# Kernel optimization log

Hardware: AMD Instinct MI355X
Metric: run time of the kernel (lower is better)

Reference implementation:

```python
import jax, jax.numpy as jnp
import numpy as np

LN_EPS = 1e-5


def layer_norm(x, g, b):
    m = jnp.mean(x, axis=-1, keepdims=True)
    v = jnp.mean(jnp.square(x - m), axis=-1, keepdims=True)
    return (x - m) * jax.lax.rsqrt(v + LN_EPS) * g + b


def sym_norm(A):
    # D^{-1/2} (A + I) D^{-1/2}
    N = A.shape[0]
    Ah = A + jnp.eye(N, dtype=A.dtype)
    d = jnp.sum(Ah, axis=-1)
    dinv = jax.lax.rsqrt(jnp.maximum(d, 1e-12))
    return Ah * dinv[:, None] * dinv[None, :]


def gru_layer(xs, Wih, Whh, bih, bhh):
    # xs: (BN, T, Din) -> ys: (BN, T, H). PyTorch GRU cell math.
    BN, T, _ = xs.shape
    H = Whh.shape[1]
    x_proj = xs @ Wih.T + bih  # (BN, T, 3H), precompute input projections

    def step(h, xp):
        hp = h @ Whh.T + bhh
        xr, xz, xn = jnp.split(xp, 3, axis=-1)
        hr, hz, hn = jnp.split(hp, 3, axis=-1)
        r = jax.nn.sigmoid(xr + hr)
        z = jax.nn.sigmoid(xz + hz)
        n = jnp.tanh(xn + r * hn)
        h_new = (1.0 - z) * n + z * h
        return h_new, h_new

    h0 = jnp.zeros((BN, H), xs.dtype)
    _, ys = jax.lax.scan(step, h0, jnp.swapaxes(x_proj, 0, 1))
    return jnp.swapaxes(ys, 0, 1)


def amscf_forward(x, A, FSP, DSP,
                  E1, E2, fus_W, fus_b, fus_v, beta1, beta2,
                  gcn_W1, gcn_b1, ln1_g, ln1_b, gcn_W2, gcn_b2, ln2_g, ln2_b,
                  gru_Wih0, gru_Whh0, gru_bih0, gru_bhh0,
                  gru_Wih1, gru_Whh1, gru_bih1, gru_bhh1,
                  att_w, fc1_W, fc1_b, fc2_W, fc2_b):
    B, T, N, _ = x.shape
    Hor = fc2_W.shape[0]

    # ImprovedAdjacency: blend A with adaptive node-embedding adjacency
    Aadp = jax.nn.softmax(jax.nn.relu(E1 @ E2.T), axis=-1)
    IA = 0.5 * A + 0.5 * Aadp

    # fuse_with_A with learned gates
    w1 = jax.nn.sigmoid(beta1)
    w2 = jax.nn.sigmoid(beta2)
    C1 = w1 * A + (1.0 - w1) * FSP
    C2 = w2 * A + (1.0 - w2) * DSP

    # TransposeAttentionFusion: graph-level attention over the 3 candidate graphs
    Gs = jnp.stack([IA, C1, C2], axis=0)  # (3, N, N)
    sc = jnp.mean(jnp.tanh(Gs @ fus_W.T + fus_b) @ fus_v, axis=-1)  # (3,)
    alpha = jax.nn.softmax(sc)
    MG = jnp.einsum('k,knm->nm', alpha, Gs)

    S_hat = sym_norm(MG)  # (N, N)

    # TwoLayerGCN over all (B, T) at once: act(LN(S X W1)) -> LN(S h W2)
    xf = x.reshape(B * T, N, 1)
    h = jnp.einsum('mn,bnc->bmc', S_hat, xf) @ gcn_W1 + gcn_b1
    h = jax.nn.relu(layer_norm(h, ln1_g, ln1_b))
    g = jnp.einsum('mn,bnc->bmc', S_hat, h) @ gcn_W2 + gcn_b2
    g = layer_norm(g, ln2_g, ln2_b)  # (B*T, N, C)

    C = g.shape[-1]
    # Faithful to original: raw view of (B, T, N, C) into (B*N, T, C)
    H_seq = g.reshape(B, T, N, C).reshape(B * N, T, C)

    out = gru_layer(H_seq, gru_Wih0, gru_Whh0, gru_bih0, gru_bhh0)
    out = gru_layer(out, gru_Wih1, gru_Whh1, gru_bih1, gru_bhh1)  # (BN, T, Hg)

    # SoftAttentionPooling over time
    score = out @ att_w  # (BN, T)
    att = jax.nn.softmax(score, axis=1)
    ctx = jnp.einsum('bt,bth->bh', att, out)

    hfc = jax.nn.gelu(ctx @ fc1_W.T + fc1_b)
    dlt = hfc @ fc2_W.T + fc2_b  # (BN, Hor); dropout is identity at eval
    return jnp.transpose(dlt.reshape(B, N, Hor), (0, 2, 1))  # (B, Hor, N)


def setup_inputs() -> dict:
    B, T, N, Hor = 32, 12, 1000, 12
    Cin, Ch, Cout, Hg, Da, De = 1, 96, 96, 192, 32, 10
    key = jax.random.key(0)
    ks = jax.random.split(key, 32)
    f32 = jnp.float32

    def nrm(k, shape, scale):
        return jax.random.normal(k, shape, dtype=f32) * scale

    inp = {
        'x': jax.random.normal(ks[0], (B, T, N, Cin), dtype=f32),
        'A': jax.random.uniform(ks[1], (N, N), dtype=f32),
        'FSP': jax.random.uniform(ks[2], (N, N), dtype=f32),
        'DSP': jax.random.uniform(ks[3], (N, N), dtype=f32),
        'E1': nrm(ks[4], (N, De), 0.1),
        'E2': nrm(ks[5], (N, De), 0.1),
        'fus_W': nrm(ks[6], (Da, N), 1.0 / np.sqrt(N)),
        'fus_b': jnp.zeros((Da,), f32),
        'fus_v': nrm(ks[7], (Da,), 1.0 / np.sqrt(Da)),
        'beta1': jnp.float32(0.5),
        'beta2': jnp.float32(0.5),
        'gcn_W1': nrm(ks[8], (Cin, Ch), 1.0 / np.sqrt(Cin)),
        'gcn_b1': jnp.zeros((Ch,), f32),
        'ln1_g': jnp.ones((Ch,), f32),
        'ln1_b': jnp.zeros((Ch,), f32),
        'gcn_W2': nrm(ks[9], (Ch, Cout), 1.0 / np.sqrt(Ch)),
        'gcn_b2': jnp.zeros((Cout,), f32),
        'ln2_g': jnp.ones((Cout,), f32),
        'ln2_b': jnp.zeros((Cout,), f32),
        'gru_Wih0': nrm(ks[10], (3 * Hg, Cout), 1.0 / np.sqrt(Hg)),
        'gru_Whh0': nrm(ks[11], (3 * Hg, Hg), 1.0 / np.sqrt(Hg)),
        'gru_bih0': jnp.zeros((3 * Hg,), f32),
        'gru_bhh0': jnp.zeros((3 * Hg,), f32),
        'gru_Wih1': nrm(ks[12], (3 * Hg, Hg), 1.0 / np.sqrt(Hg)),
        'gru_Whh1': nrm(ks[13], (3 * Hg, Hg), 1.0 / np.sqrt(Hg)),
        'gru_bih1': jnp.zeros((3 * Hg,), f32),
        'gru_bhh1': jnp.zeros((3 * Hg,), f32),
        'att_w': nrm(ks[14], (Hg,), 1.0 / np.sqrt(Hg)),
        'fc1_W': nrm(ks[15], (Hg, Hg), 1.0 / np.sqrt(Hg)),
        'fc1_b': jnp.zeros((Hg,), f32),
        'fc2_W': nrm(ks[16], (Hor, Hg), 1.0 / np.sqrt(Hg)),
        'fc2_b': jnp.zeros((Hor,), f32),
    }
    return inp


def reference(x, A, FSP, DSP, E1, E2, fus_W, fus_b, fus_v, beta1, beta2,
              gcn_W1, gcn_b1, ln1_g, ln1_b, gcn_W2, gcn_b2, ln2_g, ln2_b,
              gru_Wih0, gru_Whh0, gru_bih0, gru_bhh0,
              gru_Wih1, gru_Whh1, gru_bih1, gru_bhh1,
              att_w, fc1_W, fc1_b, fc2_W, fc2_b):
    return amscf_forward(x, A, FSP, DSP, E1, E2, fus_W, fus_b, fus_v, beta1, beta2,
                         gcn_W1, gcn_b1, ln1_g, ln1_b, gcn_W2, gcn_b2, ln2_g, ln2_b,
                         gru_Wih0, gru_Whh0, gru_bih0, gru_bhh0,
                         gru_Wih1, gru_Whh1, gru_bih1, gru_bhh1,
                         att_w, fc1_W, fc1_b, fc2_W, fc2_b)
```

## Files before the change

kernel.cpp:

```cpp
#include <hip/hip_runtime.h>

typedef unsigned short u16;
typedef unsigned int u32;
typedef __attribute__((ext_vector_type(8))) short short8;
typedef __attribute__((ext_vector_type(4))) float float4v;

#define DEV static __device__ __forceinline__

DEV float bf2f(u16 u) { u32 x = ((u32)u) << 16; float f; __builtin_memcpy(&f, &x, 4); return f; }
DEV u16 f2bf(float f) {
  u32 u; __builtin_memcpy(&u, &f, 4);
  u = (u + 0x7fffu + ((u >> 16) & 1u)) >> 16;
  return (u16)u;
}
DEV float sigm(float x) { return 1.f / (1.f + __expf(-x)); }

DEV void gl16(const u16* g, u16* l) {
  __builtin_amdgcn_global_load_lds(
      (const __attribute__((address_space(1))) void*)g,
      (__attribute__((address_space(3))) void*)l, 16, 0, 0);
}

template <int OMODE>
__launch_bounds__(256)
__global__ void gemm_nt(const u16* __restrict__ A, int lda,
                        const u16* __restrict__ B, int ldb,
                        void* __restrict__ Cp, int ldc,
                        int M, int N, int K,
                        const float* __restrict__ bias)
{
  constexpr int PK = 40;
  __shared__ u16 As[128 * PK];
  __shared__ u16 Bs[64 * PK];

  const int tid  = threadIdx.x;
  const int m0   = blockIdx.y * 128;
  const int n0   = blockIdx.x * 64;
  const int wid  = tid >> 6;
  const int lane = tid & 63;
  const int l15  = lane & 15;
  const int quad = lane >> 4;
  const int wm   = (wid >> 1) * 64;
  const int wn   = (wid & 1) * 32;

  float4v acc[4][2];
  const float4v fz = {0.f, 0.f, 0.f, 0.f};
#pragma unroll
  for (int i = 0; i < 4; i++)
#pragma unroll
    for (int j = 0; j < 2; j++) acc[i][j] = fz;

  const int arow = tid >> 2;
  const int akc  = tid & 3;

  const int kt_count = (K + 31) / 32;
  for (int kt = 0; kt < kt_count; ++kt) {
    const int k0 = kt * 32 + akc * 8;
    const bool kok = (k0 < K);
    uint4 av0 = make_uint4(0, 0, 0, 0), av1 = av0, bv = av0;
    int ra = m0 + arow;
    if (kok && ra < M)        av0 = *(const uint4*)(A + (size_t)ra * lda + k0);
    if (kok && ra + 64 < M)   av1 = *(const uint4*)(A + (size_t)(ra + 64) * lda + k0);
    int rb = n0 + arow;
    if (kok && rb < N)        bv  = *(const uint4*)(B + (size_t)rb * ldb + k0);

    __syncthreads();
    *(uint4*)&As[arow * PK + akc * 8]        = av0;
    *(uint4*)&As[(arow + 64) * PK + akc * 8] = av1;
    *(uint4*)&Bs[arow * PK + akc * 8]        = bv;
    __syncthreads();

    short8 af[4], bfr[2];
#pragma unroll
    for (int i = 0; i < 4; i++)
      af[i] = *(const short8*)&As[(wm + i * 16 + l15) * PK + quad * 8];
#pragma unroll
    for (int j = 0; j < 2; j++)
      bfr[j] = *(const short8*)&Bs[(wn + j * 16 + l15) * PK + quad * 8];
#pragma unroll
    for (int i = 0; i < 4; i++)
#pragma unroll
      for (int j = 0; j < 2; j++)
        acc[i][j] = __builtin_amdgcn_mfma_f32_16x16x32_bf16(af[i], bfr[j], acc[i][j], 0, 0, 0);
  }

#pragma unroll
  for (int i = 0; i < 4; i++)
#pragma unroll
    for (int j = 0; j < 2; j++)
#pragma unroll
      for (int e = 0; e < 4; e++) {
        int r = m0 + wm + i * 16 + quad * 4 + e;
        int c = n0 + wn + j * 16 + l15;
        if (r < M && c < N) {
          float v = acc[i][j][e];
          if (OMODE == 0) ((float*)Cp)[(size_t)r * ldc + c] = v;
          else {
            float a = v + bias[c];
            float t = tanhf(0.7978845608028654f * (a + 0.044715f * a * a * a));
            ((float*)Cp)[(size_t)r * ldc + c] = 0.5f * a * (1.f + t);
          }
        }
      }
}

__launch_bounds__(256)
__global__ void k_bigemm(const u16* __restrict__ A,
                         const u16* __restrict__ B,
                         u16* __restrict__ Gg)
{
  __shared__ u16 As[128 * 32];
  __shared__ u16 Bs[128 * 32];
  const int tid  = threadIdx.x;
  const int bid  = blockIdx.x;
  const int xcd  = bid & 7;
  const int jj   = bid >> 3;
  const int m0   = (jj & 7) * 128;
  const int n0   = (xcd + 8 * (jj >> 3)) * 128;

  const int wid  = tid >> 6;
  const int lane = tid & 63;
  const int l15  = lane & 15;
  const int quad = lane >> 4;
  const int wm   = (wid >> 1) * 64;
  const int wn   = (wid & 1) * 64;

  const int srow = wid * 16 + (lane >> 2);
  const int skc  = (lane & 3) * 8;

  const u16* agp0 = A + (size_t)(m0 + srow) * 1024 + skc;
  const u16* agp1 = agp0 + (size_t)64 * 1024;
  const u16* bgp0 = B + (size_t)(n0 + srow) * 1024 + skc;
  const u16* bgp1 = bgp0 + (size_t)64 * 1024;
  u16* asl0 = &As[(wid * 16) * 32];
  u16* asl1 = &As[(64 + wid * 16) * 32];
  u16* bsl0 = &Bs[(wid * 16) * 32];
  u16* bsl1 = &Bs[(64 + wid * 16) * 32];

  float4v acc[4][4];
  const float4v fz = {0.f, 0.f, 0.f, 0.f};
#pragma unroll
  for (int i = 0; i < 4; i++)
#pragma unroll
    for (int j = 0; j < 4; j++) acc[i][j] = fz;

  for (int kt = 0; kt < 32; ++kt) {
    const int ko = kt * 32;
    gl16(agp0 + ko, asl0);
    gl16(agp1 + ko, asl1);
    gl16(bgp0 + ko, bsl0);
    gl16(bgp1 + ko, bsl1);
    __syncthreads();
    short8 af[4], bf[4];
#pragma unroll
    for (int i = 0; i < 4; i++)
      af[i] = *(const short8*)&As[(wm + i * 16 + l15) * 32 + quad * 8];
#pragma unroll
    for (int j = 0; j < 4; j++)
      bf[j] = *(const short8*)&Bs[(wn + j * 16 + l15) * 32 + quad * 8];
#pragma unroll
    for (int i = 0; i < 4; i++)
#pragma unroll
      for (int j = 0; j < 4; j++)
        acc[i][j] = __builtin_amdgcn_mfma_f32_16x16x32_bf16(af[i], bf[j], acc[i][j], 0, 0, 0);
    __syncthreads();
  }

#pragma unroll
  for (int i = 0; i < 4; i++)
#pragma unroll
    for (int j = 0; j < 4; j++)
#pragma unroll
      for (int e = 0; e < 4; e++) {
        int r = m0 + wm + i * 16 + quad * 4 + e;
        if (r < 1000) {
          int c = n0 + wn + j * 16 + l15;
          int rs = c / 96, cc = c - rs * 96;
          Gg[(size_t)rs * 96000 + (size_t)r * 96 + cc] = f2bf(acc[i][j][e]);
        }
      }
}

template <int KX, bool POOL>
__launch_bounds__(256)
__global__ void k_gru(const u16* __restrict__ Xin, int ldx,
                      const u16* __restrict__ Win,
                      const u16* __restrict__ Hin,
                      const u16* __restrict__ Whh,
                      const float* __restrict__ bih, const float* __restrict__ bhh,
                      u16* __restrict__ Hout,
                      const float* __restrict__ att_w, float* __restrict__ score,
                      int t0)
{
  __shared__ u16 As[128 * 32];
  __shared__ u16 Bs[96 * 32];
  const int tid  = threadIdx.x;
  const int m0   = blockIdx.y * 128;
  const int c0   = blockIdx.x * 32;
  const int wid  = tid >> 6;
  const int lane = tid & 63;
  const int l15  = lane & 15;
  const int quad = lane >> 4;
  const int wm   = wid * 32;
  const int srow = lane >> 2;
  const int skc  = (lane & 3) * 8;

  float4v aR[2][2], aZ[2][2], aXN[2][2], aHN[2][2];
  const float4v fz = {0.f, 0.f, 0.f, 0.f};
#pragma unroll
  for (int i = 0; i < 2; i++)
#pragma unroll
    for (int j = 0; j < 2; j++) { aR[i][j] = fz; aZ[i][j] = fz; aXN[i][j] = fz; aHN[i][j] = fz; }

  const int br0   = wid * 16 + srow;
  const int grow0 = (br0 >> 5) * 192 + c0 + (br0 & 31);
  const int br1   = 64 + wid * 16 + srow;
  const int grow1 = 384 + c0 + (br1 & 31);
  u16* asl0 = &As[(wid * 16) * 32];
  u16* asl1 = &As[(64 + wid * 16) * 32];
  u16* bsl0 = &Bs[(wid * 16) * 32];
  u16* bsl1 = &Bs[(64 + wid * 16) * 32];

  {
    const u16* ax0 = Xin + (size_t)(m0 + wid * 16 + srow) * ldx + skc;
    const u16* ax1 = Xin + (size_t)(m0 + 64 + wid * 16 + srow) * ldx + skc;
    const u16* bx0 = Win + (size_t)grow0 * KX + skc;
    const u16* bx1 = Win + (size_t)grow1 * KX + skc;
#pragma unroll
    for (int kt = 0; kt < KX / 32; ++kt) {
      const int ko = kt * 32;
      gl16(ax0 + ko, asl0); gl16(ax1 + ko, asl1);
      gl16(bx0 + ko, bsl0);
      if (wid < 2) gl16(bx1 + ko, bsl1);
      __syncthreads();
      short8 af[2], bR[2], bZ[2], bN[2];
#pragma unroll
      for (int i = 0; i < 2; i++)
        af[i] = *(const short8*)&As[(wm + i * 16 + l15) * 32 + quad * 8];
#pragma unroll
      for (int j = 0; j < 2; j++) {
        bR[j] = *(const short8*)&Bs[(j * 16 + l15) * 32 + quad * 8];
        bZ[j] = *(const short8*)&Bs[(32 + j * 16 + l15) * 32 + quad * 8];
        bN[j] = *(const short8*)&Bs[(64 + j * 16 + l15) * 32 + quad * 8];
      }
#pragma unroll
      for (int i = 0; i < 2; i++)
#pragma unroll
        for (int j = 0; j < 2; j++) {
          aR[i][j]  = __builtin_amdgcn_mfma_f32_16x16x32_bf16(af[i], bR[j], aR[i][j], 0, 0, 0);
          aZ[i][j]  = __builtin_amdgcn_mfma_f32_16x16x32_bf16(af[i], bZ[j], aZ[i][j], 0, 0, 0);
          aXN[i][j] = __builtin_amdgcn_mfma_f32_16x16x32_bf16(af[i], bN[j], aXN[i][j], 0, 0, 0);
        }
      __syncthreads();
    }
  }
  if (!t0) {
    const u16* ah0 = Hin + (size_t)(m0 + wid * 16 + srow) * 192 + skc;
    const u16* ah1 = Hin + (size_t)(m0 + 64 + wid * 16 + srow) * 192 + skc;
    const u16* bh0 = Whh + (size_t)grow0 * 192 + skc;
    const u16* bh1 = Whh + (size_t)grow1 * 192 + skc;
#pragma unroll
    for (int kt = 0; kt < 6; ++kt) {
      const int ko = kt * 32;
      gl16(ah0 + ko, asl0); gl16(ah1 + ko, asl1);
      gl16(bh0 + ko, bsl0);
      if (wid < 2) gl16(bh1 + ko, bsl1);
      __syncthreads();
      short8 af[2], bR[2], bZ[2], bN[2];
#pragma unroll
      for (int i = 0; i < 2; i++)
        af[i] = *(const short8*)&As[(wm + i * 16 + l15) * 32 + quad * 8];
#pragma unroll
      for (int j = 0; j < 2; j++) {
        bR[j] = *(const short8*)&Bs[(j * 16 + l15) * 32 + quad * 8];
        bZ[j] = *(const short8*)&Bs[(32 + j * 16 + l15) * 32 + quad * 8];
        bN[j] = *(const short8*)&Bs[(64 + j * 16 + l15) * 32 + quad * 8];
      }
#pragma unroll
      for (int i = 0; i < 2; i++)
#pragma unroll
        for (int j = 0; j < 2; j++) {
          aR[i][j]  = __builtin_amdgcn_mfma_f32_16x16x32_bf16(af[i], bR[j], aR[i][j], 0, 0, 0);
          aZ[i][j]  = __builtin_amdgcn_mfma_f32_16x16x32_bf16(af[i], bZ[j], aZ[i][j], 0, 0, 0);
          aHN[i][j] = __builtin_amdgcn_mfma_f32_16x16x32_bf16(af[i], bN[j], aHN[i][j], 0, 0, 0);
        }
      __syncthreads();
    }
  }

  float ps[2][4];
  if (POOL) {
#pragma unroll
    for (int i = 0; i < 2; i++)
#pragma unroll
      for (int e = 0; e < 4; e++) ps[i][e] = 0.f;
  }
#pragma unroll
  for (int j = 0; j < 2; ++j) {
    const int c = c0 + j * 16 + l15;
    const float brz = bih[c] + bhh[c];
    const float bzz = bih[192 + c] + bhh[192 + c];
    const float bxn = bih[384 + c];
    const float bhn = bhh[384 + c];
    const float aw  = POOL ? att_w[c] : 0.f;
#pragma unroll
    for (int i = 0; i < 2; ++i)
#pragma unroll
      for (int e = 0; e < 4; ++e) {
        const int row = m0 + wm + i * 16 + quad * 4 + e;
        float rg  = sigm(aR[i][j][e] + brz);
        float zg  = sigm(aZ[i][j][e] + bzz);
        float hnv = bhn + (t0 ? 0.f : aHN[i][j][e]);
        float ng  = tanhf(aXN[i][j][e] + bxn + rg * hnv);
        float hold = t0 ? 0.f : bf2f(Hin[(size_t)row * 192 + c]);
        float hnew = (1.f - zg) * ng + zg * hold;
        Hout[(size_t)row * 192 + c] = f2bf(hnew);
        if (POOL) ps[i][e] += hnew * aw;
      }
  }
  if (POOL) {
#pragma unroll
    for (int i = 0; i < 2; ++i)
#pragma unroll
      for (int e = 0; e < 4; ++e) {
        float v = ps[i][e];
        v += __shfl_xor(v, 1); v += __shfl_xor(v, 2);
        v += __shfl_xor(v, 4); v += __shfl_xor(v, 8);
        if (l15 == 0) atomicAdd(&score[m0 + wm + i * 16 + quad * 4 + e], v);
      }
  }
}

__launch_bounds__(256)
__global__ void k_pool(const u16* __restrict__ H, float* __restrict__ score,
                       float* __restrict__ Mbuf, float* __restrict__ Lbuf,
                       float* __restrict__ Nv, int t0)
{
  const int base = blockIdx.x * 1536;
  const int tid  = threadIdx.x;

  float prev[6], hnew[6], so[6], wn[6];
#pragma unroll
  for (int k = 0; k < 6; k++) {
    const int idx = base + tid + k * 256;
    const int q = idx / 192;
    const float s = score[q];
    hnew[k] = bf2f(H[idx]);
    if (t0) {
      so[k] = 0.f; wn[k] = 1.f; prev[k] = 0.f;
    } else {
      const float Mo = Mbuf[q];
      const float Mn = fmaxf(Mo, s);
      so[k] = __expf(Mo - Mn);
      wn[k] = __expf(s - Mn);
      prev[k] = Nv[idx];
    }
  }
  float Mw = 0.f, Lw = 0.f;
  int qw = -1;
  if (tid < 8) {
    qw = blockIdx.x * 8 + tid;
    const float s = score[qw];
    if (t0) { Mw = s; Lw = 1.f; }
    else {
      const float Mo = Mbuf[qw];
      const float Mn = fmaxf(Mo, s);
      Mw = Mn;
      Lw = Lbuf[qw] * __expf(Mo - Mn) + __expf(s - Mn);
    }
  }
  __syncthreads();
  if (tid < 8) { Mbuf[qw] = Mw; Lbuf[qw] = Lw; score[qw] = 0.f; }
#pragma unroll
  for (int k = 0; k < 6; k++) {
    const int idx = base + tid + k * 256;
    Nv[idx] = prev[k] * so[k] + wn[k] * hnew[k];
  }
}

__launch_bounds__(256)
__global__ void k_h2gemm(const float* __restrict__ yt, const float4* __restrict__ cwpk,
                         const u16* __restrict__ W2s, const float* __restrict__ consts,
                         u16* __restrict__ h2t)
{
  constexpr int PK = 40;
  __shared__ u16 As[128 * PK];
  __shared__ u16 Bs[96 * PK];
  __shared__ u16 Ts[96 * 136];

  const int tid  = threadIdx.x;
  const int m0   = blockIdx.x * 128;
  const int wid  = tid >> 6;
  const int lane = tid & 63;
  const int l15  = lane & 15;
  const int quad = lane >> 4;
  const int wm   = (wid >> 1) * 64;
  const int wn   = (wid & 1) * 48;

  const float P = consts[0], Q = consts[1], VW = consts[2], CWB = consts[3], VB = consts[4];

  const int arow = tid >> 2;
  const int akc  = tid & 3;

  float yv[2], mu[2], iv[2];
#pragma unroll
  for (int rr = 0; rr < 2; rr++) {
    int i = m0 + arow + rr * 64;
    int r = i / 1000, n = i - r * 1000;
    float y = yt[n * 384 + r];
    yv[rr] = y;
    mu[rr] = y * P + Q;
    iv[rr] = rsqrtf(y * y * VW + 2.f * y * CWB + VB + 1e-5f);
  }

  float4v acc[4][3];
  const float4v fz = {0.f, 0.f, 0.f, 0.f};
#pragma unroll
  for (int i = 0; i < 4; i++)
#pragma unroll
    for (int j = 0; j < 3; j++) acc[i][j] = fz;

  uint4 asave[2][3];
  const bool has2 = (arow < 32);

  for (int kt = 0; kt < 6; ++kt) {
    const int k0 = kt * 32 + akc * 8;
    uint4 av[2];
    if (kt < 3) {
#pragma unroll
      for (int rr = 0; rr < 2; rr++) {
        u16 hb[8];
#pragma unroll
        for (int e = 0; e < 8; e++) {
          float4 cw = cwpk[k0 + e];
          float t = yv[rr] * cw.x + cw.y - mu[rr];
          float h = fmaxf(t * iv[rr] * cw.z + cw.w, 0.f);
          hb[e] = f2bf(h);
        }
        __builtin_memcpy(&av[rr], hb, 16);
        asave[rr][kt] = av[rr];
      }
    } else {
      av[0] = asave[0][kt - 3];
      av[1] = asave[1][kt - 3];
    }
    uint4 bv0 = *(const uint4*)(W2s + (size_t)arow * 192 + k0);
    uint4 bv1 = make_uint4(0, 0, 0, 0);
    if (has2) bv1 = *(const uint4*)(W2s + (size_t)(arow + 64) * 192 + k0);

    __syncthreads();
    *(uint4*)&As[arow * PK + akc * 8]        = av[0];
    *(uint4*)&As[(arow + 64) * PK + akc * 8] = av[1];
    *(uint4*)&Bs[arow * PK + akc * 8]        = bv0;
    if (has2) *(uint4*)&Bs[(arow + 64) * PK + akc * 8] = bv1;
    __syncthreads();

    short8 af[4], bfr[3];
#pragma unroll
    for (int i = 0; i < 4; i++)
      af[i] = *(const short8*)&As[(wm + i * 16 + l15) * PK + quad * 8];
#pragma unroll
    for (int j = 0; j < 3; j++)
      bfr[j] = *(const short8*)&Bs[(wn + j * 16 + l15) * PK + quad * 8];
#pragma unroll
    for (int i = 0; i < 4; i++)
#pragma unroll
      for (int j = 0; j < 3; j++)
        acc[i][j] = __builtin_amdgcn_mfma_f32_16x16x32_bf16(af[i], bfr[j], acc[i][j], 0, 0, 0);
  }

#pragma unroll
  for (int i = 0; i < 4; i++)
#pragma unroll
    for (int j = 0; j < 3; j++)
#pragma unroll
      for (int e = 0; e < 4; e++) {
        int rowl = wm + i * 16 + quad * 4 + e;
        int c2   = wn + j * 16 + l15;
        Ts[c2 * 136 + rowl] = f2bf(acc[i][j][e]);
      }
  __syncthreads();
#pragma unroll
  for (int u = tid; u < 1536; u += 256) {
    int c2 = u >> 4, ch = u & 15;
    int iidx0 = m0 + ch * 8;
    int r = iidx0 / 1000, n0 = iidx0 - r * 1000;
    *(uint4*)(h2t + (size_t)(r * 96 + c2) * 1024 + n0) = *(const uint4*)&Ts[c2 * 136 + ch * 8];
  }
}

__launch_bounds__(256)
__global__ void k_prep(const float* x, const float* fus_W,
                       const float* Wih0, const float* Whh0,
                       const float* Wih1, const float* Whh1,
                       const float* gcn_W1, const float* gcn_b1,
                       const float* gcn_W2, const float* ln1g, const float* ln1b,
                       u16* xbf, u16* fusWbf, u16* Wih0b, u16* Whh0b, u16* Wih1b, u16* Whh1b,
                       u16* W2s, float4* cwpk, float* consts)
{
  long o = (long)blockIdx.x * 256 + threadIdx.x;
  if (o < 384000) xbf[o] = f2bf(x[o]);
  else if ((o -= 384000) < 32000) fusWbf[o] = f2bf(fus_W[o]);
  else if ((o -= 32000) < 55296)  Wih0b[o] = f2bf(Wih0[o]);
  else if ((o -= 55296) < 110592) Whh0b[o] = f2bf(Whh0[o]);
  else if ((o -= 110592) < 110592) Wih1b[o] = f2bf(Wih1[o]);
  else if ((o -= 110592) < 110592) Whh1b[o] = f2bf(Whh1[o]);
  else if ((o -= 110592) < 9216) {
    int c2 = (int)o / 96, c = (int)o - c2 * 96;
    float wv = gcn_W2[c * 96 + c2];
    u16 hi = f2bf(wv);
    u16 lo = f2bf(wv - bf2f(hi));
    W2s[c2 * 192 + c] = hi;
    W2s[c2 * 192 + 96 + c] = lo;
  }
  else if ((o -= 9216) < 96) {
    int c = (int)o;
    float4 cw;
    cw.x = gcn_W1[c]; cw.y = gcn_b1[c]; cw.z = ln1g[c]; cw.w = ln1b[c];
    cwpk[c] = cw;
  }
  if (blockIdx.x == 0 && threadIdx.x == 0) {
    float sw = 0, sb = 0, sww = 0, swb = 0, sbb = 0;
    for (int c = 0; c < 96; c++) {
      float wv = gcn_W1[c], b = gcn_b1[c];
      sw += wv; sb += b; sww += wv * wv; swb += wv * b; sbb += b * b;
    }
    float P = sw / 96.f, Q = sb / 96.f;
    consts[0] = P; consts[1] = Q;
    consts[2] = sww / 96.f - P * P;
    consts[3] = swb / 96.f - P * Q;
    consts[4] = sbb / 96.f - Q * Q;
  }
}

__launch_bounds__(256)
__global__ void k_zero(u16* __restrict__ h2t, float* __restrict__ score)
{
  int idx = blockIdx.x * 256 + threadIdx.x;
  if (idx < 110592) {
    int row = idx / 3, p = idx - row * 3;
    *(uint4*)(h2t + (size_t)row * 1024 + 1000 + p * 8) = make_uint4(0, 0, 0, 0);
  } else if ((idx -= 110592) < 32000) {
    score[idx] = 0.f;
  }
}

__launch_bounds__(256)
__global__ void k_w1split(const float* __restrict__ fc1W, u16* __restrict__ w1s)
{
  int idx = blockIdx.x * 256 + threadIdx.x;
  if (idx >= 192 * 192) return;
  int n = idx / 192, k = idx - n * 192;
  float w = fc1W[idx];
  u16 hi = f2bf(w);
  u16 lo = f2bf(w - bf2f(hi));
  w1s[(size_t)n * 576 + k]       = hi;
  w1s[(size_t)n * 576 + 192 + k] = lo;
  w1s[(size_t)n * 576 + 384 + k] = hi;
}

__launch_bounds__(256)
__global__ void k_adjrow(const float* __restrict__ A, const float* __restrict__ FSP,
                         const float* __restrict__ DSP, const float* __restrict__ E1,
                         const float* __restrict__ E2,
                         const float* beta1, const float* beta2,
                         u16* __restrict__ G, float* __restrict__ rowsums)
{
  __shared__ float z[1000];
  __shared__ float red[256];
  const int n = blockIdx.x, tid = threadIdx.x;

  float e1r[10];
#pragma unroll
  for (int d = 0; d < 10; d++) e1r[d] = E1[n * 10 + d];

  float lmax = -1e30f;
  for (int m = tid; m < 1000; m += 256) {
    float s = 0;
#pragma unroll
    for (int d = 0; d < 10; d++) s += e1r[d] * E2[m * 10 + d];
    s = fmaxf(s, 0.f);
    z[m] = s;
    lmax = fmaxf(lmax, s);
  }
  red[tid] = lmax; __syncthreads();
  for (int st = 128; st > 0; st >>= 1) { if (tid < st) red[tid] = fmaxf(red[tid], red[tid + st]); __syncthreads(); }
  const float mx = red[0]; __syncthreads();

  float lsum = 0;
  for (int m = tid; m < 1000; m += 256) { float e = __expf(z[m] - mx); z[m] = e; lsum += e; }
  red[tid] = lsum; __syncthreads();
  for (int st = 128; st > 0; st >>= 1) { if (tid < st) red[tid] += red[tid + st]; __syncthreads(); }
  const float inv = 1.f / red[0]; __syncthreads();

  const float w1 = sigm(beta1[0]);
  const float w2 = sigm(beta2[0]);
  float s0 = 0, s1 = 0, s2 = 0;
  for (int m = tid; m < 1000; m += 256) {
    float aadp = z[m] * inv;
    float a = A[n * 1000 + m], f = FSP[n * 1000 + m], dd = DSP[n * 1000 + m];
    float g0 = 0.5f * a + 0.5f * aadp;
    float g1 = w1 * a + (1.f - w1) * f;
    float g2 = w2 * a + (1.f - w2) * dd;
    G[0 * 1000000 + n * 1000 + m] = f2bf(g0);
    G[1 * 1000000 + n * 1000 + m] = f2bf(g1);
    G[2 * 1000000 + n * 1000 + m] = f2bf(g2);
    s0 += g0; s1 += g1; s2 += g2;
  }
  red[tid] = s0; __syncthreads();
  for (int st = 128; st > 0; st >>= 1) { if (tid < st) red[tid] += red[tid + st]; __syncthreads(); }
  if (tid == 0) rowsums[n] = red[0];
  __syncthreads();
  red[tid] = s1; __syncthreads();
  for (int st = 128; st > 0; st >>= 1) { if (tid < st) red[tid] += red[tid + st]; __syncthreads(); }
  if (tid == 0) rowsums[1000 + n] = red[0];
  __syncthreads();
  red[tid] = s2; __syncthreads();
  for (int st = 128; st > 0; st >>= 1) { if (tid < st) red[tid] += red[tid + st]; __syncthreads(); }
  if (tid == 0) rowsums[2000 + n] = red[0];
}

__launch_bounds__(256)
__global__ void k_sc(const float* __restrict__ P, const float* fus_b, const float* fus_v, float* sc)
{
  __shared__ float red[256];
  const int k = blockIdx.x, tid = threadIdx.x;
  float local = 0;
  for (int n = tid; n < 1000; n += 256) {
    const float* p = P + (size_t)(k * 1000 + n) * 32;
    float s = 0;
#pragma unroll
    for (int a = 0; a < 32; a++) s += tanhf(p[a] + fus_b[a]) * fus_v[a];
    local += s;
  }
  red[tid] = local; __syncthreads();
  for (int st = 128; st > 0; st >>= 1) { if (tid < st) red[tid] += red[tid + st]; __syncthreads(); }
  if (tid == 0) sc[k] = red[0] * (1.f / 1000.f);
}

__launch_bounds__(256)
__global__ void k_alpha(const float* sc, const float* rowsums, float* alpha_out, float* dinv)
{
  __shared__ float al[3];
  const int tid = threadIdx.x;
  if (tid == 0) {
    float m = fmaxf(sc[0], fmaxf(sc[1], sc[2]));
    float e0 = __expf(sc[0] - m), e1 = __expf(sc[1] - m), e2 = __expf(sc[2] - m);
    float inv = 1.f / (e0 + e1 + e2);
    al[0] = e0 * inv; al[1] = e1 * inv; al[2] = e2 * inv;
    alpha_out[0] = al[0]; alpha_out[1] = al[1]; alpha_out[2] = al[2];
  }
  __syncthreads();
  const float a0 = al[0], a1 = al[1], a2 = al[2];
  for (int n = tid; n < 1000; n += 256) {
    float d = a0 * rowsums[n] + a1 * rowsums[1000 + n] + a2 * rowsums[2000 + n] + 1.0f;
    dinv[n] = rsqrtf(fmaxf(d, 1e-12f));
  }
}

__launch_bounds__(256)
__global__ void k_shat(const u16* __restrict__ G, const float* alpha, const float* dinv,
                       u16* __restrict__ S)
{
  int idx = blockIdx.x * 256 + threadIdx.x;
  if (idx >= 1024000) return;
  int i = idx >> 10, j = idx & 1023;
  u16 val = 0;
  if (j < 1000) {
    const float a0 = alpha[0], a1 = alpha[1], a2 = alpha[2];
    int g = i * 1000 + j;
    float mg = a0 * bf2f(G[g]) + a1 * bf2f(G[1000000 + g]) + a2 * bf2f(G[2000000 + g]);
    if (i == j) mg += 1.0f;
    val = f2bf(mg * dinv[i] * dinv[j]);
  }
  S[(size_t)i * 1024 + j] = val;
}

__launch_bounds__(256)
__global__ void k_ln2g(u16* __restrict__ g, const float* __restrict__ b2,
                       const float* __restrict__ g2, const float* __restrict__ be2)
{
  const int i = blockIdx.x * 256 + threadIdx.x;
  if (i >= 384000) return;
  u16* row = g + (size_t)i * 96;

  uint4 raw[12];
#pragma unroll
  for (int t = 0; t < 12; t++) raw[t] = *(const uint4*)((const u16*)row + t * 8);

  float s = 0, ss = 0;
#pragma unroll
  for (int t = 0; t < 12; t++) {
    const u16* ch = (const u16*)&raw[t];
#pragma unroll
    for (int e = 0; e < 8; e++) {
      float v = bf2f(ch[e]) + b2[t * 8 + e];
      s += v; ss += v * v;
    }
  }
  const float mean = s * (1.f / 96.f);
  const float var  = ss * (1.f / 96.f) - mean * mean;
  const float isd  = rsqrtf(var + 1e-5f);

#pragma unroll
  for (int t = 0; t < 12; t++) {
    const u16* ch = (const u16*)&raw[t];
#pragma unroll
    for (int p = 0; p < 2; p++) {
      int c0 = t * 8 + p * 4;
      u32 w0 = f2bf((bf2f(ch[p * 4 + 0]) + b2[c0 + 0] - mean) * isd * g2[c0 + 0] + be2[c0 + 0]);
      u32 w1 = f2bf((bf2f(ch[p * 4 + 1]) + b2[c0 + 1] - mean) * isd * g2[c0 + 1] + be2[c0 + 1]);
      u32 w2 = f2bf((bf2f(ch[p * 4 + 2]) + b2[c0 + 2] - mean) * isd * g2[c0 + 2] + be2[c0 + 2]);
      u32 w3 = f2bf((bf2f(ch[p * 4 + 3]) + b2[c0 + 3] - mean) * isd * g2[c0 + 3] + be2[c0 + 3]);
      ((u32*)row)[t * 4 + p * 2 + 0] = (w0 | (w1 << 16));
      ((u32*)row)[t * 4 + p * 2 + 1] = (w2 | (w3 << 16));
    }
  }
}

__launch_bounds__(256)
__global__ void k_ctxsplit(const float* __restrict__ Nv, const float* __restrict__ Lbuf,
                           u16* __restrict__ ctxs)
{
  const int i = blockIdx.x * 256 + threadIdx.x;
  if (i >= 32000 * 192) return;
  const int q = i / 192, c = i - q * 192;
  float v = Nv[i] / Lbuf[q];
  u16 hi = f2bf(v);
  u16 lo = f2bf(v - bf2f(hi));
  u16* row = ctxs + (size_t)q * 576;
  row[c] = hi; row[192 + c] = hi; row[384 + c] = lo;
}

__launch_bounds__(192)
__global__ void k_fc2(const float* __restrict__ hfc, const float* __restrict__ fc2W,
                      const float* __restrict__ fc2b, float* __restrict__ out)
{
  __shared__ float w2S[12][193];
  __shared__ float hS[16][193];
  const int tid = threadIdx.x;
  const int q0 = blockIdx.x * 16;
  for (int idx = tid; idx < 12 * 192; idx += 192) {
    int o = idx / 192, k = idx - o * 192;
    w2S[o][k] = fc2W[idx];
  }
  for (int idx = tid; idx < 16 * 192; idx += 192) {
    int qq = idx / 192, k = idx - qq * 192;
    hS[qq][k] = hfc[(size_t)(q0 + qq) * 192 + k];
  }
  __syncthreads();
  const int qq = tid / 12, o = tid - qq * 12;
  float acc = fc2b[o];
#pragma unroll 8
  for (int k = 0; k < 192; k++) acc += hS[qq][k] * w2S[o][k];
  const int q = q0 + qq;
  const int b = q / 1000, node = q - b * 1000;
  out[(size_t)b * 12000 + o * 1000 + node] = acc;
}

extern "C" void kernel_launch(void* const* d_in, const int* in_sizes, int n_in,
                              void* d_out, int out_size, void* d_ws, size_t ws_size,
                              hipStream_t stream)
{
  const float* x     = (const float*)d_in[0];
  const float* A     = (const float*)d_in[1];
  const float* FSP   = (const float*)d_in[2];
  const float* DSP   = (const float*)d_in[3];
  const float* E1    = (const float*)d_in[4];
  const float* E2    = (const float*)d_in[5];
  const float* fus_W = (const float*)d_in[6];
  const float* fus_b = (const float*)d_in[7];
  const float* fus_v = (const float*)d_in[8];
  const float* beta1 = (const float*)d_in[9];
  const float* beta2 = (const float*)d_in[10];
  const float* gcn_W1= (const float*)d_in[11];
  const float* gcn_b1= (const float*)d_in[12];
  const float* ln1g  = (const float*)d_in[13];
  const float* ln1b  = (const float*)d_in[14];
  const float* gcn_W2= (const float*)d_in[15];
  const float* gcn_b2= (const float*)d_in[16];
  const float* ln2g  = (const float*)d_in[17];
  const float* ln2b  = (const float*)d_in[18];
  const float* Wih0  = (const float*)d_in[19];
  const float* Whh0  = (const float*)d_in[20];
  const float* bih0  = (const float*)d_in[21];
  const float* bhh0  = (const float*)d_in[22];
  const float* Wih1  = (const float*)d_in[23];
  const float* Whh1  = (const float*)d_in[24];
  const float* bih1  = (const float*)d_in[25];
  const float* bhh1  = (const float*)d_in[26];
  const float* att_w = (const float*)d_in[27];
  const float* fc1W  = (const float*)d_in[28];
  const float* fc1b  = (const float*)d_in[29];
  const float* fc2W  = (const float*)d_in[30];
  const float* fc2b  = (const float*)d_in[31];
  float* out = (float*)d_out;

  char* w = (char*)d_ws;
  auto alloc = [&](size_t bytes) -> char* {
    char* p = w;
    w += (bytes + 255) & ~(size_t)255;
    return p;
  };

  float* consts  = (float*)alloc(8 * 4);
  float* scp     = (float*)alloc(3 * 4);
  float* alphap  = (float*)alloc(3 * 4);
  float* rowsums = (float*)alloc(3000 * 4);
  float* dinvp   = (float*)alloc(1000 * 4);
  u16*   Gbuf    = (u16*)alloc((size_t)3000000 * 2);
  u16*   Sbf     = (u16*)alloc((size_t)1024 * 1024 * 2);
  u16*   xbf     = (u16*)alloc((size_t)384000 * 2);
  u16*   fusWbf  = (u16*)alloc((size_t)32000 * 2);
  u16*   Wih0b   = (u16*)alloc((size_t)55296 * 2);
  u16*   Whh0b   = (u16*)alloc((size_t)110592 * 2);
  u16*   Wih1b   = (u16*)alloc((size_t)110592 * 2);
  u16*   Whh1b   = (u16*)alloc((size_t)110592 * 2);
  u16*   w1s     = (u16*)alloc((size_t)192 * 576 * 2);
  u16*   W2s     = (u16*)alloc((size_t)96 * 192 * 2);
  float4* cwpk   = (float4*)alloc((size_t)96 * 16);
  float* Pbuf    = (float*)alloc((size_t)96000 * 4);
  float* yt      = (float*)alloc((size_t)384000 * 4);
  u16*   h2t     = (u16*)alloc((size_t)36864 * 1024 * 2);
  u16*   Gg      = (u16*)alloc((size_t)36864000 * 2);
  float* Nv      = (float*)alloc((size_t)6144000 * 4);
  float* Mbuf    = (float*)alloc((size_t)32000 * 4);
  float* Lbuf    = (float*)alloc((size_t)32000 * 4);
  float* score   = (float*)alloc((size_t)32000 * 4);

  u16* h0buf[2] = { h2t,                    h2t + (size_t)6144000 };
  u16* h1buf[2] = { h2t + (size_t)12288000, h2t + (size_t)18432000 };
  u16*   ctxs = h2t;
  float* hfc  = (float*)(h2t + (size_t)18432000);

  k_prep<<<3174, 256, 0, stream>>>(x, fus_W, Wih0, Whh0, Wih1, Whh1, gcn_W1, gcn_b1,
                                   gcn_W2, ln1g, ln1b,
                                   xbf, fusWbf, Wih0b, Whh0b, Wih1b, Whh1b, W2s, cwpk, consts);
  k_w1split<<<144, 256, 0, stream>>>(fc1W, w1s);
  k_zero<<<557, 256, 0, stream>>>(h2t, score);
  k_adjrow<<<1000, 256, 0, stream>>>(A, FSP, DSP, E1, E2, beta1, beta2, Gbuf, rowsums);
  gemm_nt<0><<<dim3(1, 24), 256, 0, stream>>>(Gbuf, 1000, fusWbf, 1000, Pbuf, 32, 3000, 32, 1000, nullptr);
  k_sc<<<3, 256, 0, stream>>>(Pbuf, fus_b, fus_v, scp);
  k_alpha<<<1, 256, 0, stream>>>(scp, rowsums, alphap, dinvp);
  k_shat<<<4000, 256, 0, stream>>>(Gbuf, alphap, dinvp, Sbf);
  gemm_nt<0><<<dim3(6, 8), 256, 0, stream>>>(Sbf, 1024, xbf, 1000, yt, 384, 1000, 384, 1000, nullptr);
  k_h2gemm<<<3000, 256, 0, stream>>>(yt, cwpk, W2s, consts, h2t);
  k_bigemm<<<2304, 256, 0, stream>>>(Sbf, h2t, Gg);
  k_ln2g<<<1500, 256, 0, stream>>>(Gg, gcn_b2, ln2g, ln2b);

  for (int t = 0; t < 12; ++t) {
    u16* h0in  = h0buf[t & 1];
    u16* h0out = h0buf[(t & 1) ^ 1];
    u16* h1in  = h1buf[t & 1];
    u16* h1out = h1buf[(t & 1) ^ 1];
    k_gru<96, false><<<dim3(6, 250), 256, 0, stream>>>(
        Gg + t * 96, 1152, Wih0b, h0in, Whh0b, bih0, bhh0, h0out, nullptr, nullptr, t == 0);
    k_gru<192, true><<<dim3(6, 250), 256, 0, stream>>>(
        h0out, 192, Wih1b, h1in, Whh1b, bih1, bhh1, h1out, att_w, score, t == 0);
    k_pool<<<4000, 256, 0, stream>>>(h1out, score, Mbuf, Lbuf, Nv, t == 0);
  }

  k_ctxsplit<<<24000, 256, 0, stream>>>(Nv, Lbuf, ctxs);
  gemm_nt<3><<<dim3(3, 250), 256, 0, stream>>>(ctxs, 576, w1s, 576, hfc, 192, 32000, 192, 576, fc1b);
  k_fc2<<<2000, 192, 0, stream>>>(hfc, fc2W, fc2b, out);
}
```

Baseline: 1.651 ms.

## Swizzle LDS tiles and widen GRU K-tiles to 64 to cut bank conflicts

Applies an XOR swizzle to the LDS column placement in the big GEMM and in the GRU kernel, so the MFMA fragment reads spread across banks instead of conflicting. For the 192-wide inputs and the hidden-state GEMMs in the GRU, the K tile grows from 32 to 64 with an 8-way swizzle. This halves the number of barrier-separated load stages, at the cost of larger LDS buffers, which may reduce occupancy. The GRU step kernel is launched once per timestep, so per-step latency dominates the total time.

```diff
diff --git a/kernel.cpp b/kernel.cpp
--- a/kernel.cpp
+++ b/kernel.cpp
@@ -126,7 +126,7 @@
   const int wn   = (wid & 1) * 64;
 
   const int srow = wid * 16 + (lane >> 2);
-  const int skc  = (lane & 3) * 8;
+  const int skc  = (((lane & 3) ^ ((lane >> 2) & 3))) * 8;
 
   const u16* agp0 = A + (size_t)(m0 + srow) * 1024 + skc;
   const u16* agp1 = agp0 + (size_t)64 * 1024;
@@ -144,6 +144,8 @@
 #pragma unroll
     for (int j = 0; j < 4; j++) acc[i][j] = fz;
 
+  const int swa = (quad ^ (l15 & 3)) * 8;
+
   for (int kt = 0; kt < 32; ++kt) {
     const int ko = kt * 32;
     gl16(agp0 + ko, asl0);
@@ -154,10 +156,10 @@
     short8 af[4], bf[4];
 #pragma unroll
     for (int i = 0; i < 4; i++)
-      af[i] = *(const short8*)&As[(wm + i * 16 + l15) * 32 + quad * 8];
+      af[i] = *(const short8*)&As[(wm + i * 16 + l15) * 32 + swa];
 #pragma unroll
     for (int j = 0; j < 4; j++)
-      bf[j] = *(const short8*)&Bs[(wn + j * 16 + l15) * 32 + quad * 8];
+      bf[j] = *(const short8*)&Bs[(wn + j * 16 + l15) * 32 + swa];
 #pragma unroll
     for (int i = 0; i < 4; i++)
 #pragma unroll
@@ -192,8 +194,8 @@
                       const float* __restrict__ att_w, float* __restrict__ score,
                       int t0)
 {
-  __shared__ u16 As[128 * 32];
-  __shared__ u16 Bs[96 * 32];
+  __shared__ u16 As[128 * 64];
+  __shared__ u16 Bs[96 * 64];
   const int tid  = threadIdx.x;
   const int m0   = blockIdx.y * 128;
   const int c0   = blockIdx.x * 32;
@@ -202,8 +204,11 @@
   const int l15  = lane & 15;
   const int quad = lane >> 4;
   const int wm   = wid * 32;
-  const int srow = lane >> 2;
-  const int skc  = (lane & 3) * 8;
+
+  const int srow8 = lane >> 3;
+  const int sw8   = ((lane & 7) ^ srow8) * 8;
+  const int srow4 = lane >> 2;
+  const int sw4   = (((lane & 3) ^ (srow4 & 3))) * 8;
 
   float4v aR[2][2], aZ[2][2], aXN[2][2], aHN[2][2];
   const float4v fz = {0.f, 0.f, 0.f, 0.f};
@@ -212,22 +217,20 @@
 #pragma unroll
     for (int j = 0; j < 2; j++) { aR[i][j] = fz; aZ[i][j] = fz; aXN[i][j] = fz; aHN[i][j] = fz; }
 
-  const int br0   = wid * 16 + srow;
-  const int grow0 = (br0 >> 5) * 192 + c0 + (br0 & 31);
-  const int br1   = 64 + wid * 16 + srow;
-  const int grow1 = 384 + c0 + (br1 & 31);
-  u16* asl0 = &As[(wid * 16) * 32];
-  u16* asl1 = &As[(64 + wid * 16) * 32];
-  u16* bsl0 = &Bs[(wid * 16) * 32];
-  u16* bsl1 = &Bs[(64 + wid * 16) * 32];
-
-  {
-    const u16* ax0 = Xin + (size_t)(m0 + wid * 16 + srow) * ldx + skc;
-    const u16* ax1 = Xin + (size_t)(m0 + 64 + wid * 16 + srow) * ldx + skc;
-    const u16* bx0 = Win + (size_t)grow0 * KX + skc;
-    const u16* bx1 = Win + (size_t)grow1 * KX + skc;
-#pragma unroll
-    for (int kt = 0; kt < KX / 32; ++kt) {
+  if (KX == 96) {
+    const u16* ax0 = Xin + (size_t)(m0 + wid * 16 + srow4) * ldx + sw4;
+    const u16* ax1 = Xin + (size_t)(m0 + 64 + wid * 16 + srow4) * ldx + sw4;
+    const int b0 = wid * 16 + srow4;
+    const u16* bx0 = Win + (size_t)((b0 >> 5) * 192 + c0 + (b0 & 31)) * 96 + sw4;
+    const int b1 = 64 + wid * 16 + srow4;
+    const u16* bx1 = Win + (size_t)(384 + c0 + (b1 & 31)) * 96 + sw4;
+    u16* asl0 = &As[(wid * 16) * 32];
+    u16* asl1 = &As[(64 + wid * 16) * 32];
+    u16* bsl0 = &Bs[(wid * 16) * 32];
+    u16* bsl1 = &Bs[(64 + wid * 16) * 32];
+    const int swa = (quad ^ (l15 & 3)) * 8;
+#pragma unroll
+    for (int kt = 0; kt < 3; ++kt) {
       const int ko = kt * 32;
       gl16(ax0 + ko, asl0); gl16(ax1 + ko, asl1);
       gl16(bx0 + ko, bsl0);
@@ -236,12 +239,12 @@
       short8 af[2], bR[2], bZ[2], bN[2];
 #pragma unroll
       for (int i = 0; i < 2; i++)
-        af[i] = *(const short8*)&As[(wm + i * 16 + l15) * 32 + quad * 8];
+        af[i] = *(const short8*)&As[(wm + i * 16 + l15) * 32 + swa];
 #pragma unroll
       for (int j = 0; j < 2; j++) {
-        bR[j] = *(const short8*)&Bs[(j * 16 + l15) * 32 + quad * 8];
-        bZ[j] = *(const short8*)&Bs[(32 + j * 16 + l15) * 32 + quad * 8];
-        bN[j] = *(const short8*)&Bs[(64 + j * 16 + l15) * 32 + quad * 8];
+        bR[j] = *(const short8*)&Bs[(j * 16 + l15) * 32 + swa];
+        bZ[j] = *(const short8*)&Bs[(32 + j * 16 + l15) * 32 + swa];
+        bN[j] = *(const short8*)&Bs[(64 + j * 16 + l15) * 32 + swa];
       }
 #pragma unroll
       for (int i = 0; i < 2; i++)
@@ -253,37 +256,79 @@
         }
       __syncthreads();
     }
+  } else {
+    const u16* abase = Xin + (size_t)(m0 + wid * 8 + srow8) * 192 + sw8;
+    const u16* bbase = Win + (size_t)(c0 + wid * 8 + srow8) * 192 + sw8;
+#pragma unroll
+    for (int kt = 0; kt < 3; ++kt) {
+      const int ko = kt * 64;
+#pragma unroll
+      for (int c = 0; c < 4; c++)
+        gl16(abase + (size_t)c * 32 * 192 + ko, &As[(c * 32 + wid * 8) * 64]);
+#pragma unroll
+      for (int c = 0; c < 3; c++)
+        gl16(bbase + (size_t)c * 192 * 192 + ko, &Bs[(c * 32 + wid * 8) * 64]);
+      __syncthreads();
+#pragma unroll
+      for (int k32 = 0; k32 < 2; k32++) {
+        const int swr = ((quad + 4 * k32) ^ (l15 & 7)) * 8;
+        short8 af[2], bR[2], bZ[2], bN[2];
+#pragma unroll
+        for (int i = 0; i < 2; i++)
+          af[i] = *(const short8*)&As[(wm + i * 16 + l15) * 64 + swr];
+#pragma unroll
+        for (int j = 0; j < 2; j++) {
+          bR[j] = *(const short8*)&Bs[(j * 16 + l15) * 64 + swr];
+          bZ[j] = *(const short8*)&Bs[(32 + j * 16 + l15) * 64 + swr];
+          bN[j] = *(const short8*)&Bs[(64 + j * 16 + l15) * 64 + swr];
+        }
+#pragma unroll
+        for (int i = 0; i < 2; i++)
+#pragma unroll
+          for (int j = 0; j < 2; j++) {
+            aR[i][j]  = __builtin_amdgcn_mfma_f32_16x16x32_bf16(af[i], bR[j], aR[i][j], 0, 0, 0);
+            aZ[i][j]  = __builtin_amdgcn_mfma_f32_16x16x32_bf16(af[i], bZ[j], aZ[i][j], 0, 0, 0);
+            aXN[i][j] = __builtin_amdgcn_mfma_f32_16x16x32_bf16(af[i], bN[j], aXN[i][j], 0, 0, 0);
+          }
+      }
+      __syncthreads();
+    }
   }
   if (!t0) {
-    const u16* ah0 = Hin + (size_t)(m0 + wid * 16 + srow) * 192 + skc;
-    const u16* ah1 = Hin + (size_t)(m0 + 64 + wid * 16 + srow) * 192 + skc;
-    const u16* bh0 = Whh + (size_t)grow0 * 192 + skc;
-    const u16* bh1 = Whh + (size_t)grow1 * 192 + skc;
-#pragma unroll
-    for (int kt = 0; kt < 6; ++kt) {
-      const int ko = kt * 32;
-      gl16(ah0 + ko, asl0); gl16(ah1 + ko, asl1);
-      gl16(bh0 + ko, bsl0);
-      if (wid < 2) gl16(bh1 + ko, bsl1);
+    const u16* abase = Hin + (size_t)(m0 + wid * 8 + srow8) * 192 + sw8;
+    const u16* bbase = Whh + (size_t)(c0 + wid * 8 + srow8) * 192 + sw8;
+#pragma unroll
+    for (int kt = 0; kt < 3; ++kt) {
+      const int ko = kt * 64;
+#pragma unroll
+      for (int c = 0; c < 4; c++)
+        gl16(abase + (size_t)c * 32 * 192 + ko, &As[(c * 32 + wid * 8) * 64]);
+#pragma unroll
+      for (int c = 0; c < 3; c++)
+        gl16(bbase + (size_t)c * 192 * 192 + ko, &Bs[(c * 32 + wid * 8) * 64]);
       __syncthreads();
-      short8 af[2], bR[2], bZ[2], bN[2];
-#pragma unroll
-      for (int i = 0; i < 2; i++)
-        af[i] = *(const short8*)&As[(wm + i * 16 + l15) * 32 + quad * 8];
-#pragma unroll
-      for (int j = 0; j < 2; j++) {
-        bR[j] = *(const short8*)&Bs[(j * 16 + l15) * 32 + quad * 8];
-        bZ[j] = *(const short8*)&Bs[(32 + j * 16 + l15) * 32 + quad * 8];
-        bN[j] = *(const short8*)&Bs[(64 + j * 16 + l15) * 32 + quad * 8];
+#pragma unroll
+      for (int k32 = 0; k32 < 2; k32++) {
+        const int swr = ((quad + 4 * k32) ^ (l15 & 7)) * 8;
+        short8 af[2], bR[2], bZ[2], bN[2];
+#pragma unroll
+        for (int i = 0; i < 2; i++)
+          af[i] = *(const short8*)&As[(wm + i * 16 + l15) * 64 + swr];
+#pragma unroll
+        for (int j = 0; j < 2; j++) {
+          bR[j] = *(const short8*)&Bs[(j * 16 + l15) * 64 + swr];
+          bZ[j] = *(const short8*)&Bs[(32 + j * 16 + l15) * 64 + swr];
+          bN[j] = *(const short8*)&Bs[(64 + j * 16 + l15) * 64 + swr];
+        }
+#pragma unroll
+        for (int i = 0; i < 2; i++)
+#pragma unroll
+          for (int j = 0; j < 2; j++) {
+            aR[i][j]  = __builtin_amdgcn_mfma_f32_16x16x32_bf16(af[i], bR[j], aR[i][j], 0, 0, 0);
+            aZ[i][j]  = __builtin_amdgcn_mfma_f32_16x16x32_bf16(af[i], bZ[j], aZ[i][j], 0, 0, 0);
+            aHN[i][j] = __builtin_amdgcn_mfma_f32_16x16x32_bf16(af[i], bN[j], aHN[i][j], 0, 0, 0);
+          }
       }
-#pragma unroll
-      for (int i = 0; i < 2; i++)
-#pragma unroll
-        for (int j = 0; j < 2; j++) {
-          aR[i][j]  = __builtin_amdgcn_mfma_f32_16x16x32_bf16(af[i], bR[j], aR[i][j], 0, 0, 0);
-          aZ[i][j]  = __builtin_amdgcn_mfma_f32_16x16x32_bf16(af[i], bZ[j], aZ[i][j], 0, 0, 0);
-          aHN[i][j] = __builtin_amdgcn_mfma_f32_16x16x32_bf16(af[i], bN[j], aHN[i][j], 0, 0, 0);
-        }
       __syncthreads();
     }
   }
```

New measurement: 1.512 ms. 8.4% less time.
